# Optimization experiments

Measured on AMD Instinct MI355X. Metric: run time of the kernel, lower is better.

## Reference

```python
import jax, jax.numpy as jnp
import numpy as np

N, D_IN, D_HID, D_OUT = 16384, 512, 2048, 512
NUM_BANDS, RANK, ALPHA = 4, 16, 32
SCALING = ALPHA / RANK  # 2.0


def setup_inputs() -> dict:
    key = jax.random.key(0)
    ks = jax.random.split(key, 10)
    x = jax.random.normal(ks[0], (N, D_IN), dtype=jnp.float32)
    bw = jax.random.uniform(ks[1], (N, NUM_BANDS), dtype=jnp.float32)
    band_weights = bw / jnp.sum(bw, axis=-1, keepdims=True)  # rows sum to 1
    s_in = 1.0 / np.sqrt(D_IN)
    s_hid = 1.0 / np.sqrt(D_HID)
    return {
        "x": x,
        "band_weights": band_weights,
        "W1": jax.random.normal(ks[2], (D_IN, D_HID), dtype=jnp.float32) * s_in,
        "b1": jax.random.normal(ks[3], (D_HID,), dtype=jnp.float32) * 0.01,
        "W2": jax.random.normal(ks[4], (D_HID, D_OUT), dtype=jnp.float32) * s_hid,
        "b2": jax.random.normal(ks[5], (D_OUT,), dtype=jnp.float32) * 0.01,
        "lora_fc1_A": jax.random.normal(ks[6], (NUM_BANDS, D_IN, RANK), dtype=jnp.float32) * s_in,
        "lora_fc1_B": jax.random.normal(ks[7], (NUM_BANDS, RANK, D_HID), dtype=jnp.float32) * 0.02,
        "lora_fc2_A": jax.random.normal(ks[8], (NUM_BANDS, D_HID, RANK), dtype=jnp.float32) * s_hid,
        "lora_fc2_B": jax.random.normal(ks[9], (NUM_BANDS, RANK, D_OUT), dtype=jnp.float32) * 0.02,
    }


def reference(x, band_weights, W1, b1, W2, b2, lora_fc1_A, lora_fc1_B, lora_fc2_A, lora_fc2_B):
    # shared fc1: [N, hidden]
    h_shared = x @ W1 + b1
    # per-band LoRA down-projection: [N, bands, rank]
    t1 = jnp.einsum('ni,bir->nbr', x, lora_fc1_A)
    # up-project and band-weighted sum fused: [N, hidden]
    delta1 = jnp.einsum('nb,nbr,brh->nh', band_weights, t1, lora_fc1_B) * SCALING
    h = jax.nn.gelu(h_shared + delta1, approximate=False)  # torch GELU is erf-based
    out_shared = h @ W2 + b2
    t2 = jnp.einsum('nh,bhr->nbr', h, lora_fc2_A)
    delta2 = jnp.einsum('nb,nbr,bro->no', band_weights, t2, lora_fc2_B) * SCALING
    return out_shared + delta2
```

## Files before the change

### kernel.cpp

```cpp
#include <hip/hip_runtime.h>
#include <hip/hip_bf16.h>

#define DEV __device__ __forceinline__
#define AS1 __attribute__((address_space(1)))
#define AS3 __attribute__((address_space(3)))

typedef __attribute__((ext_vector_type(8))) short bf16x8;
typedef __attribute__((ext_vector_type(4))) float f32x4;

static constexpr int NR   = 16384;
static constexpr int DIN  = 512;
static constexpr int DHID = 2048;
static constexpr int DOUT = 512;
static constexpr int LR   = 64;
static constexpr int K1   = DIN + LR;
static constexpr int K2   = DHID + LR;

DEV unsigned short f2bf(float f) {
  unsigned u = __float_as_uint(f);
  u += 0x7fffu + ((u >> 16) & 1u);
  return (unsigned short)(u >> 16);
}

DEV float fast_gelu(float v) {
  float x2 = v * v;
  float a  = -v * __builtin_fmaf(0.10294324f, x2, 2.30220817f);
  float t  = exp2f(a);
  return v * __builtin_amdgcn_rcpf(1.0f + t);
}

template<int N> DEV void wvm() {
  asm volatile("s_waitcnt vmcnt(%0)" :: "i"(N) : "memory");
}

__global__ __launch_bounds__(256) void cvt_x_kernel(const float* __restrict__ x,
                                                    unsigned short* __restrict__ xaug) {
  int i = blockIdx.x * 256 + threadIdx.x;
  if (i >= NR * DIN / 4) return;
  int e = i * 4;
  int r = e >> 9, c = e & 511;
  float4 v = ((const float4*)x)[i];
  uint2 o;
  o.x = (unsigned)f2bf(v.x) | ((unsigned)f2bf(v.y) << 16);
  o.y = (unsigned)f2bf(v.z) | ((unsigned)f2bf(v.w) << 16);
  *(uint2*)(xaug + (size_t)r * K1 + c) = o;
}

template<int R, int C, int LDO, int CO>
__global__ __launch_bounds__(256) void tconv_kernel(const float* __restrict__ in,
                                                    unsigned short* __restrict__ out) {
  __shared__ float t[32][33];
  int bc = blockIdx.x * 32, br = blockIdx.y * 32;
  int tx = threadIdx.x & 31, ty = threadIdx.x >> 5;
  #pragma unroll
  for (int i = 0; i < 32; i += 8)
    t[ty + i][tx] = in[(size_t)(br + ty + i) * C + bc + tx];
  __syncthreads();
  #pragma unroll
  for (int i = 0; i < 32; i += 8)
    out[(size_t)(bc + ty + i) * LDO + CO + br + tx] = f2bf(t[tx][ty + i]);
}

__global__ __launch_bounds__(256) void rearrA_kernel(const float* __restrict__ A,
                                                     unsigned short* __restrict__ AT, int D) {
  int tid = blockIdx.x * 256 + threadIdx.x;
  if (tid >= 64 * D) return;
  int j = tid / D, i = tid - j * D;
  AT[tid] = f2bf(A[((size_t)(j >> 4) * D + i) * 16 + (j & 15)]);
}

template<int BM, int BN, int WAVES, int K, int EPI>
__global__ __launch_bounds__(WAVES * 64, 2) void gemm8_kernel(
    const unsigned short* __restrict__ A, int lda,
    const unsigned short* __restrict__ B, int ldb,
    const float* __restrict__ bias,
    void* __restrict__ outp, int ldo, int ocol) {
  constexpr int THREADS = WAVES * 64;
  constexpr int NT = K / 64;
  constexpr int AL = BM * 4 / THREADS;
  constexpr int BL = BN * 4 / THREADS;
  constexpr int HA = (BM / 2) * 64;
  constexpr int HB = (BN / 2) * 64;
  constexpr int MQ = BM / 64;
  constexpr int WC = WAVES / 2;
  static_assert(NT >= 2, "K tiles");
  __shared__ __align__(16) unsigned short lA[4 * HA];
  __shared__ __align__(16) unsigned short lB[4 * HB];

  const int tid  = threadIdx.x;
  const int w    = tid >> 6, lane = tid & 63;
  const int wr   = w / WC, wc = w % WC;
  const int bm   = blockIdx.x * BM, bn = blockIdx.y * BN;
  const int l15  = lane & 15;
  const int kc0  = ((lane >> 4) ^ (lane & 7)) * 8;
  const int kc1  = (((lane >> 4) + 4) ^ (lane & 7)) * 8;

  f32x4 acc[2][2][MQ][2] = {};
  bf16x8 af[MQ][2];
  bf16x8 bfv[2][2][2];

  auto stageA = [&](int buf, int half, int t) {
    #pragma unroll
    for (int i = 0; i < AL; ++i) {
      int row = w * (AL * 8) + i * 8 + (lane >> 3);
      __builtin_amdgcn_global_load_lds(
          (const AS1 void*)(A + (size_t)(bm + half * (BM / 2) + row) * lda
                              + (size_t)t * 64 + (((lane & 7) ^ (row & 7)) * 8)),
          (AS3 void*)(lA + (buf * 2 + half) * HA + (w * AL + i) * 512),
          16, 0, 0);
    }
  };
  auto stageB = [&](int buf, int half, int t) {
    #pragma unroll
    for (int i = 0; i < BL; ++i) {
      int row = w * (BL * 8) + i * 8 + (lane >> 3);
      __builtin_amdgcn_global_load_lds(
          (const AS1 void*)(B + (size_t)(bn + half * (BN / 2) + row) * ldb
                              + (size_t)t * 64 + (((lane & 7) ^ (row & 7)) * 8)),
          (AS3 void*)(lB + (buf * 2 + half) * HB + (w * BL + i) * 512),
          16, 0, 0);
    }
  };
  auto ldA = [&](int buf, int mh) {
    const unsigned short* sA = lA + (buf * 2 + mh) * HA;
    #pragma unroll
    for (int m = 0; m < MQ; ++m) {
      int ro = (wr * (BM / 4) + m * 16 + l15) * 64;
      af[m][0] = *(const bf16x8*)(sA + ro + kc0);
      af[m][1] = *(const bf16x8*)(sA + ro + kc1);
    }
  };
  auto ldB = [&](int buf, int nh) {
    const unsigned short* sB = lB + (buf * 2 + nh) * HB;
    #pragma unroll
    for (int n = 0; n < 2; ++n) {
      int ro = (wc * 32 + n * 16 + l15) * 64;
      bfv[nh][n][0] = *(const bf16x8*)(sB + ro + kc0);
      bfv[nh][n][1] = *(const bf16x8*)(sB + ro + kc1);
    }
  };

#define MFMA_Q(mh, nh)                                                           \
  __builtin_amdgcn_s_setprio(1);                                                 \
  _Pragma("unroll")                                                              \
  for (int m = 0; m < MQ; ++m)                                                   \
    _Pragma("unroll")                                                            \
    for (int n = 0; n < 2; ++n) {                                                \
      acc[mh][nh][m][n] = __builtin_amdgcn_mfma_f32_16x16x32_bf16(               \
          af[m][0], bfv[nh][n][0], acc[mh][nh][m][n], 0, 0, 0);                  \
      acc[mh][nh][m][n] = __builtin_amdgcn_mfma_f32_16x16x32_bf16(               \
          af[m][1], bfv[nh][n][1], acc[mh][nh][m][n], 0, 0, 0);                  \
    }                                                                            \
  __builtin_amdgcn_s_setprio(0);

  stageA(0, 0, 0); stageB(0, 0, 0); stageB(0, 1, 0); stageA(0, 1, 0);
  wvm<0>();
  __builtin_amdgcn_s_barrier();

  for (int t = 0; t < NT; ++t) {
    const int buf = t & 1, nb = buf ^ 1;
    const bool more = (t + 1 < NT);
    ldA(buf, 0);
    ldB(buf, 0);
    if (more) {
      stageA(nb, 0, t + 1); stageB(nb, 0, t + 1);
      stageB(nb, 1, t + 1); stageA(nb, 1, t + 1);
    }
    MFMA_Q(0, 0);
    ldB(buf, 1);
    MFMA_Q(0, 1);
    ldA(buf, 1);
    MFMA_Q(1, 1);
    MFMA_Q(1, 0);
    wvm<0>();
    __builtin_amdgcn_s_barrier();
  }
#undef MFMA_Q

  float biasv[2][2];
  #pragma unroll
  for (int nh = 0; nh < 2; ++nh)
    #pragma unroll
    for (int n = 0; n < 2; ++n)
      biasv[nh][n] = bias[bn + nh * (BN / 2) + wc * 32 + n * 16 + l15];

  #pragma unroll
  for (int mh = 0; mh < 2; ++mh)
    #pragma unroll
    for (int nh = 0; nh < 2; ++nh)
      #pragma unroll
      for (int m = 0; m < MQ; ++m)
        #pragma unroll
        for (int n = 0; n < 2; ++n) {
          int col  = bn + nh * (BN / 2) + wc * 32 + n * 16 + l15;
          int rowb = bm + mh * (BM / 2) + wr * (BM / 4) + m * 16 + ((lane >> 4) << 2);
          #pragma unroll
          for (int r = 0; r < 4; ++r) {
            float v = acc[mh][nh][m][n][r];
            int row = rowb + r;
            if (EPI == 0) {
              v = fast_gelu(v + biasv[nh][n]);
              ((unsigned short*)outp)[(size_t)row * ldo + ocol + col] = f2bf(v);
            } else {
              v += biasv[nh][n];
              ((float*)outp)[(size_t)row * ldo + col] = v;
            }
          }
        }
}

template<int BM, int BN, int WM, int WN, int K>
__global__ __launch_bounds__(256) void gemmu_kernel(
    const unsigned short* __restrict__ A, int lda,
    const unsigned short* __restrict__ B, int ldb,
    const float* __restrict__ bw,
    unsigned short* __restrict__ outp, int ldo, int ocol) {
  constexpr int WRM = WM / 16, WRN = WN / 16;
  constexpr int NWN = BN / WN;
  constexpr int NT  = K / 32;
  constexpr int NBUF = 3;
  constexpr int AISS = BM / 64;
  constexpr int BISS = BN / 64;
  constexpr int LOADS = AISS + BISS;
  static_assert((BM / WM) * (BN / WN) == 4, "4 waves");
  __shared__ __align__(16) unsigned short lA[NBUF * BM * 32];
  __shared__ __align__(16) unsigned short lB[NBUF * BN * 32];

  const int tid  = threadIdx.x;
  const int wid  = tid >> 6, lane = tid & 63;
  const int wr   = wid / NWN, wc = wid % NWN;
  const int bm   = blockIdx.x * BM, bn = blockIdx.y * BN;
  const int srow = lane >> 2;
  const int scol = (((lane & 3) ^ ((lane >> 2) & 3)) * 8);
  const int kch  = (((lane >> 4) ^ (lane & 3)) * 8);

  f32x4 acc[WRM][WRN] = {};

  auto stage = [&](int buf, int t) {
    #pragma unroll
    for (int i = 0; i < AISS; i++) {
      int row = i * 64 + wid * 16 + srow;
      __builtin_amdgcn_global_load_lds(
          (const AS1 void*)(A + (size_t)(bm + row) * lda + t * 32 + scol),
          (AS3 void*)(lA + buf * (BM * 32) + i * 2048 + wid * 512), 16, 0, 0);
    }
    #pragma unroll
    for (int i = 0; i < BISS; i++) {
      int row = i * 64 + wid * 16 + srow;
      __builtin_amdgcn_global_load_lds(
          (const AS1 void*)(B + (size_t)(bn + row) * ldb + t * 32 + scol),
          (AS3 void*)(lB + buf * (BN * 32) + i * 2048 + wid * 512), 16, 0, 0);
    }
  };
  auto compute = [&](int buf) {
    const unsigned short* pA = lA + buf * (BM * 32);
    const unsigned short* pB = lB + buf * (BN * 32);
    bf16x8 af[WRM], bfv[WRN];
    #pragma unroll
    for (int m = 0; m < WRM; m++)
      af[m] = *(const bf16x8*)(pA + (wr * WM + m * 16 + (lane & 15)) * 32 + kch);
    #pragma unroll
    for (int n = 0; n < WRN; n++)
      bfv[n] = *(const bf16x8*)(pB + (wc * WN + n * 16 + (lane & 15)) * 32 + kch);
    #pragma unroll
    for (int m = 0; m < WRM; m++)
      #pragma unroll
      for (int n = 0; n < WRN; n++)
        acc[m][n] = __builtin_amdgcn_mfma_f32_16x16x32_bf16(af[m], bfv[n], acc[m][n], 0, 0, 0);
  };

  stage(0, 0); stage(1, 1); stage(2, 2);
  wvm<2 * LOADS>();
  __builtin_amdgcn_s_barrier();

  int bt = 0;
  for (int t = 0; t < NT; ++t) {
    compute(bt);
    __builtin_amdgcn_s_barrier();
    if (t + 1 < NT) {
      if (t + NBUF < NT) stage(bt, t + NBUF);
      int newer = (t + NBUF < NT) ? (NBUF - 1) : (NT - 2 - t);
      if (newer >= 2)      wvm<2 * LOADS>();
      else if (newer == 1) wvm<LOADS>();
      else                 wvm<0>();
      __builtin_amdgcn_s_barrier();
      bt = (bt == NBUF - 1) ? 0 : bt + 1;
    }
  }

  const int r0 = bm + wr * WM;
  const int c0 = bn + wc * WN;
  #pragma unroll
  for (int m = 0; m < WRM; m++)
    #pragma unroll
    for (int n = 0; n < WRN; n++) {
      int col  = c0 + n * 16 + (lane & 15);
      int rowb = r0 + m * 16 + ((lane >> 4) << 2);
      #pragma unroll
      for (int r = 0; r < 4; r++) {
        float v = acc[m][n][r] * 2.0f * bw[(rowb + r) * 4 + (col >> 4)];
        outp[(size_t)(rowb + r) * ldo + ocol + col] = f2bf(v);
      }
    }
}

extern "C" void kernel_launch(void* const* d_in, const int* in_sizes, int n_in,
                              void* d_out, int out_size, void* d_ws, size_t ws_size,
                              hipStream_t stream) {
  const float* x  = (const float*)d_in[0];
  const float* bw = (const float*)d_in[1];
  const float* W1 = (const float*)d_in[2];
  const float* b1 = (const float*)d_in[3];
  const float* W2 = (const float*)d_in[4];
  const float* b2 = (const float*)d_in[5];
  const float* A1 = (const float*)d_in[6];
  const float* B1 = (const float*)d_in[7];
  const float* A2 = (const float*)d_in[8];
  const float* B2 = (const float*)d_in[9];
  float* out = (float*)d_out;

  char* w = (char*)d_ws;
  unsigned short* xaug = (unsigned short*)w;  w += (size_t)NR * K1 * 2;
  unsigned short* haug = (unsigned short*)w;  w += (size_t)NR * K2 * 2;
  unsigned short* W1cT = (unsigned short*)w;  w += (size_t)DHID * K1 * 2;
  unsigned short* W2cT = (unsigned short*)w;  w += (size_t)DOUT * K2 * 2;
  unsigned short* A1T  = (unsigned short*)w;  w += (size_t)64 * DIN * 2;
  unsigned short* A2T  = (unsigned short*)w;  w += (size_t)64 * DHID * 2;

  cvt_x_kernel<<<NR * DIN / 4 / 256, 256, 0, stream>>>(x, xaug);
  tconv_kernel<512, 2048, K1, 0><<<dim3(64, 16), 256, 0, stream>>>(W1, W1cT);
  tconv_kernel<64, 2048, K1, 512><<<dim3(64, 2), 256, 0, stream>>>(B1, W1cT);
  tconv_kernel<2048, 512, K2, 0><<<dim3(16, 64), 256, 0, stream>>>(W2, W2cT);
  tconv_kernel<64, 512, K2, 2048><<<dim3(16, 2), 256, 0, stream>>>(B2, W2cT);
  rearrA_kernel<<<128, 256, 0, stream>>>(A1, A1T, 512);
  rearrA_kernel<<<512, 256, 0, stream>>>(A2, A2T, 2048);

  gemmu_kernel<64, 64, 32, 32, 512><<<dim3(NR / 64, 1), 256, 0, stream>>>(
      xaug, K1, A1T, DIN, bw, xaug, K1, 512);
  gemm8_kernel<256, 256, 8, K1, 0><<<dim3(NR / 256, DHID / 256), 512, 0, stream>>>(
      xaug, K1, W1cT, K1, b1, haug, K2, 0);
  gemmu_kernel<64, 64, 32, 32, 2048><<<dim3(NR / 64, 1), 256, 0, stream>>>(
      haug, K2, A2T, DHID, bw, haug, K2, 2048);
  gemm8_kernel<128, 128, 4, K2, 1><<<dim3(NR / 128, DOUT / 128), 256, 0, stream>>>(
      haug, K2, W2cT, K2, b2, out, DOUT, 0);
}
```

Before: 147.3 us.

## Rework gemm8 into a finer-grained staged pipeline with 8 waves and 256-row tiles

The gemm8 kernel is restructured around a fixed 512-thread, 256-row block with a configurable wave grid (MW). The main loop is unrolled by two K tiles and interleaves half-tile global-to-LDS loads with the MFMA quadrants, using barriers between each phase. B for the next tile is prefetched early and waits are partial (vmcnt of 2*BL), so loads can overlap compute instead of waiting for everything each iteration. The fc2 GEMM moves from 128x128 tiles with 4 waves to 256x128 tiles with 8 waves, which doubles reuse of B per block but halves the block count and adds many more barriers.

```diff
diff --git a/kernel.cpp b/kernel.cpp
--- a/kernel.cpp
+++ b/kernel.cpp
@@ -69,42 +69,48 @@
   AT[tid] = f2bf(A[((size_t)(j >> 4) * D + i) * 16 + (j & 15)]);
 }
 
-template<int BM, int BN, int WAVES, int K, int EPI>
-__global__ __launch_bounds__(WAVES * 64, 2) void gemm8_kernel(
+template<int BM, int BN, int MW, int K, int EPI>
+__global__ __launch_bounds__(512, 2) void gemm8_kernel(
     const unsigned short* __restrict__ A, int lda,
     const unsigned short* __restrict__ B, int ldb,
     const float* __restrict__ bias,
     void* __restrict__ outp, int ldo, int ocol) {
-  constexpr int THREADS = WAVES * 64;
-  constexpr int NT = K / 64;
-  constexpr int AL = BM * 4 / THREADS;
-  constexpr int BL = BN * 4 / THREADS;
-  constexpr int HA = (BM / 2) * 64;
-  constexpr int HB = (BN / 2) * 64;
-  constexpr int MQ = BM / 64;
-  constexpr int WC = WAVES / 2;
-  static_assert(NT >= 2, "K tiles");
-  __shared__ __align__(16) unsigned short lA[4 * HA];
-  __shared__ __align__(16) unsigned short lB[4 * HB];
+  constexpr int NW  = 8 / MW;
+  constexpr int WMR = BM / MW, WNC = BN / NW;
+  constexpr int QR  = WMR / 2, QC = WNC / 2;
+  constexpr int MQ  = QR / 16, NQ = QC / 16;
+  constexpr int AL  = 2;
+  constexpr int BL  = BN / 128;
+  constexpr int HA  = 128 * 64;
+  constexpr int HB  = (BN / 2) * 64;
+  constexpr int NT  = K / 64;
+  constexpr int NJ  = NT / 2;
+  static_assert(BM == 256 && NT >= 3, "geometry");
+  __shared__ __align__(16) unsigned short lA[2 * 2 * HA];
+  __shared__ __align__(16) unsigned short lB[2 * 2 * HB];
 
   const int tid  = threadIdx.x;
   const int w    = tid >> 6, lane = tid & 63;
-  const int wr   = w / WC, wc = w % WC;
+  const int wr   = w / NW, wc = w % NW;
+  const int ah   = wr / (MW / 2);
+  const int rloc = (wr % (MW / 2)) * WMR;
+  const int bh   = wc / (NW / 2);
+  const int cloc = (wc % (NW / 2)) * WNC;
   const int bm   = blockIdx.x * BM, bn = blockIdx.y * BN;
   const int l15  = lane & 15;
   const int kc0  = ((lane >> 4) ^ (lane & 7)) * 8;
   const int kc1  = (((lane >> 4) + 4) ^ (lane & 7)) * 8;
 
-  f32x4 acc[2][2][MQ][2] = {};
+  f32x4 acc[2][2][MQ][NQ] = {};
   bf16x8 af[MQ][2];
-  bf16x8 bfv[2][2][2];
+  bf16x8 bfv[2][NQ][2];
 
   auto stageA = [&](int buf, int half, int t) {
     #pragma unroll
     for (int i = 0; i < AL; ++i) {
-      int row = w * (AL * 8) + i * 8 + (lane >> 3);
+      int row = (w * AL + i) * 8 + (lane >> 3);
       __builtin_amdgcn_global_load_lds(
-          (const AS1 void*)(A + (size_t)(bm + half * (BM / 2) + row) * lda
+          (const AS1 void*)(A + (size_t)(bm + half * 128 + row) * lda
                               + (size_t)t * 64 + (((lane & 7) ^ (row & 7)) * 8)),
           (AS3 void*)(lA + (buf * 2 + half) * HA + (w * AL + i) * 512),
           16, 0, 0);
@@ -113,7 +119,7 @@
   auto stageB = [&](int buf, int half, int t) {
     #pragma unroll
     for (int i = 0; i < BL; ++i) {
-      int row = w * (BL * 8) + i * 8 + (lane >> 3);
+      int row = (w * BL + i) * 8 + (lane >> 3);
       __builtin_amdgcn_global_load_lds(
           (const AS1 void*)(B + (size_t)(bn + half * (BN / 2) + row) * ldb
                               + (size_t)t * 64 + (((lane & 7) ^ (row & 7)) * 8)),
@@ -121,88 +127,127 @@
           16, 0, 0);
     }
   };
-  auto ldA = [&](int buf, int mh) {
-    const unsigned short* sA = lA + (buf * 2 + mh) * HA;
+  auto ldA = [&](int buf, int qm) {
+    const unsigned short* sA = lA + (buf * 2 + ah) * HA;
     #pragma unroll
     for (int m = 0; m < MQ; ++m) {
-      int ro = (wr * (BM / 4) + m * 16 + l15) * 64;
+      int ro = (rloc + qm * QR + m * 16 + l15) * 64;
       af[m][0] = *(const bf16x8*)(sA + ro + kc0);
       af[m][1] = *(const bf16x8*)(sA + ro + kc1);
     }
   };
-  auto ldB = [&](int buf, int nh) {
-    const unsigned short* sB = lB + (buf * 2 + nh) * HB;
-    #pragma unroll
-    for (int n = 0; n < 2; ++n) {
-      int ro = (wc * 32 + n * 16 + l15) * 64;
-      bfv[nh][n][0] = *(const bf16x8*)(sB + ro + kc0);
-      bfv[nh][n][1] = *(const bf16x8*)(sB + ro + kc1);
-    }
-  };
-
-#define MFMA_Q(mh, nh)                                                           \
+  auto ldB = [&](int buf, int qn) {
+    const unsigned short* sB = lB + (buf * 2 + bh) * HB;
+    #pragma unroll
+    for (int n = 0; n < NQ; ++n) {
+      int ro = (cloc + qn * QC + n * 16 + l15) * 64;
+      bfv[qn][n][0] = *(const bf16x8*)(sB + ro + kc0);
+      bfv[qn][n][1] = *(const bf16x8*)(sB + ro + kc1);
+    }
+  };
+
+#define MFMA_Q(qm, qn)                                                           \
   __builtin_amdgcn_s_setprio(1);                                                 \
   _Pragma("unroll")                                                              \
   for (int m = 0; m < MQ; ++m)                                                   \
     _Pragma("unroll")                                                            \
-    for (int n = 0; n < 2; ++n) {                                                \
-      acc[mh][nh][m][n] = __builtin_amdgcn_mfma_f32_16x16x32_bf16(               \
-          af[m][0], bfv[nh][n][0], acc[mh][nh][m][n], 0, 0, 0);                  \
-      acc[mh][nh][m][n] = __builtin_amdgcn_mfma_f32_16x16x32_bf16(               \
-          af[m][1], bfv[nh][n][1], acc[mh][nh][m][n], 0, 0, 0);                  \
+    for (int n = 0; n < NQ; ++n) {                                               \
+      acc[qm][qn][m][n] = __builtin_amdgcn_mfma_f32_16x16x32_bf16(               \
+          af[m][0], bfv[qn][n][0], acc[qm][qn][m][n], 0, 0, 0);                  \
+      acc[qm][qn][m][n] = __builtin_amdgcn_mfma_f32_16x16x32_bf16(               \
+          af[m][1], bfv[qn][n][1], acc[qm][qn][m][n], 0, 0, 0);                  \
     }                                                                            \
   __builtin_amdgcn_s_setprio(0);
 
-  stageA(0, 0, 0); stageB(0, 0, 0); stageB(0, 1, 0); stageA(0, 1, 0);
-  wvm<0>();
-  __builtin_amdgcn_s_barrier();
-
-  for (int t = 0; t < NT; ++t) {
-    const int buf = t & 1, nb = buf ^ 1;
-    const bool more = (t + 1 < NT);
-    ldA(buf, 0);
-    ldB(buf, 0);
-    if (more) {
-      stageA(nb, 0, t + 1); stageB(nb, 0, t + 1);
-      stageB(nb, 1, t + 1); stageA(nb, 1, t + 1);
-    }
+#define BAR() __builtin_amdgcn_s_barrier()
+
+  stageB(0, 0, 0); stageB(0, 1, 0); stageA(0, 0, 0); stageA(0, 1, 0);
+  stageB(1, 0, 1); stageB(1, 1, 1);
+  wvm<2 * BL>();
+  BAR();
+
+  for (int j = 0; j < NJ; ++j) {
+    const int T1 = 2 * j + 1, T2 = 2 * j + 2, T3 = 2 * j + 3;
+    ldA(0, 0); ldB(0, 0);
+    stageA(1, 0, T1);
+    BAR();
     MFMA_Q(0, 0);
-    ldB(buf, 1);
+    BAR();
+    ldB(0, 1);
+    stageA(1, 1, T1);
+    BAR();
     MFMA_Q(0, 1);
-    ldA(buf, 1);
+    BAR();
+    ldA(0, 1);
+    if (T2 < NT) stageB(0, 0, T2);
+    BAR();
+    MFMA_Q(1, 1);
+    BAR();
+    if (T2 < NT) stageB(0, 1, T2);
+    BAR();
+    MFMA_Q(1, 0);
+    if (T2 < NT) wvm<2 * BL>(); else wvm<0>();
+    BAR();
+    ldA(1, 0); ldB(1, 0);
+    if (T2 < NT) stageA(0, 0, T2);
+    BAR();
+    MFMA_Q(0, 0);
+    BAR();
+    ldB(1, 1);
+    if (T2 < NT) stageA(0, 1, T2);
+    BAR();
+    MFMA_Q(0, 1);
+    BAR();
+    ldA(1, 1);
+    if (T3 < NT) stageB(1, 0, T3);
+    BAR();
+    MFMA_Q(1, 1);
+    BAR();
+    if (T3 < NT) stageB(1, 1, T3);
+    BAR();
+    MFMA_Q(1, 0);
+    if (T3 < NT) wvm<2 * BL>(); else wvm<0>();
+    BAR();
+  }
+
+  if (NT & 1) {
+    ldA(0, 0); ldB(0, 0);
+    MFMA_Q(0, 0);
+    ldB(0, 1);
+    MFMA_Q(0, 1);
+    ldA(0, 1);
     MFMA_Q(1, 1);
     MFMA_Q(1, 0);
-    wvm<0>();
-    __builtin_amdgcn_s_barrier();
   }
 #undef MFMA_Q
-
-  float biasv[2][2];
-  #pragma unroll
-  for (int nh = 0; nh < 2; ++nh)
-    #pragma unroll
-    for (int n = 0; n < 2; ++n)
-      biasv[nh][n] = bias[bn + nh * (BN / 2) + wc * 32 + n * 16 + l15];
-
-  #pragma unroll
-  for (int mh = 0; mh < 2; ++mh)
-    #pragma unroll
-    for (int nh = 0; nh < 2; ++nh)
+#undef BAR
+
+  float biasv[2][NQ];
+  #pragma unroll
+  for (int qn = 0; qn < 2; ++qn)
+    #pragma unroll
+    for (int n = 0; n < NQ; ++n)
+      biasv[qn][n] = bias[bn + bh * (BN / 2) + cloc + qn * QC + n * 16 + l15];
+
+  #pragma unroll
+  for (int qm = 0; qm < 2; ++qm)
+    #pragma unroll
+    for (int qn = 0; qn < 2; ++qn)
       #pragma unroll
       for (int m = 0; m < MQ; ++m)
         #pragma unroll
-        for (int n = 0; n < 2; ++n) {
-          int col  = bn + nh * (BN / 2) + wc * 32 + n * 16 + l15;
-          int rowb = bm + mh * (BM / 2) + wr * (BM / 4) + m * 16 + ((lane >> 4) << 2);
+        for (int n = 0; n < NQ; ++n) {
+          int col  = bn + bh * (BN / 2) + cloc + qn * QC + n * 16 + l15;
+          int rowb = bm + ah * 128 + rloc + qm * QR + m * 16 + ((lane >> 4) << 2);
           #pragma unroll
           for (int r = 0; r < 4; ++r) {
-            float v = acc[mh][nh][m][n][r];
+            float v = acc[qm][qn][m][n][r];
             int row = rowb + r;
             if (EPI == 0) {
-              v = fast_gelu(v + biasv[nh][n]);
+              v = fast_gelu(v + biasv[qn][n]);
               ((unsigned short*)outp)[(size_t)row * ldo + ocol + col] = f2bf(v);
             } else {
-              v += biasv[nh][n];
+              v += biasv[qn][n];
               ((float*)outp)[(size_t)row * ldo + col] = v;
             }
           }
@@ -337,10 +382,10 @@
 
   gemmu_kernel<64, 64, 32, 32, 512><<<dim3(NR / 64, 1), 256, 0, stream>>>(
       xaug, K1, A1T, DIN, bw, xaug, K1, 512);
-  gemm8_kernel<256, 256, 8, K1, 0><<<dim3(NR / 256, DHID / 256), 512, 0, stream>>>(
+  gemm8_kernel<256, 256, 2, K1, 0><<<dim3(NR / 256, DHID / 256), 512, 0, stream>>>(
       xaug, K1, W1cT, K1, b1, haug, K2, 0);
   gemmu_kernel<64, 64, 32, 32, 2048><<<dim3(NR / 64, 1), 256, 0, stream>>>(
       haug, K2, A2T, DHID, bw, haug, K2, 2048);
-  gemm8_kernel<128, 128, 4, K2, 1><<<dim3(NR / 128, DOUT / 128), 256, 0, stream>>>(
+  gemm8_kernel<256, 128, 4, K2, 1><<<dim3(NR / 256, DOUT / 128), 512, 0, stream>>>(
       haug, K2, W2cT, K2, b2, out, DOUT, 0);
 }
```

New measurement: 150.6 us. +2.2%, slower.

## Split main GEMM K-loop into two barrier phases and widen LoRA GEMM K-tile

Applied to the files above, without the earlier changes.

The main GEMM loop now loads all A fragments up front and computes the nh=0 quadrants first. Partial vmcnt waits and a mid-iteration barrier let the last B half-tile be staged later, so global-to-LDS loads overlap more with MFMA work instead of draining at the end of each tile. The LoRA down-projection GEMM moves from 32-wide to 64-wide K tiles with an XOR-swizzled LDS layout, giving two MFMAs per fragment pair and half as many pipeline iterations. This costs more registers for A fragments and twice the LDS for the triple-buffered LoRA kernel, which may reduce occupancy.

```diff
diff --git a/kernel.cpp b/kernel.cpp
--- a/kernel.cpp
+++ b/kernel.cpp
@@ -70,7 +70,7 @@
 }
 
 template<int BM, int BN, int WAVES, int K, int EPI>
-__global__ __launch_bounds__(WAVES * 64, 2) void gemm8_kernel(
+__global__ __launch_bounds__(WAVES * 64, 2) void gemmx_kernel(
     const unsigned short* __restrict__ A, int lda,
     const unsigned short* __restrict__ B, int ldb,
     const float* __restrict__ bias,
@@ -83,7 +83,7 @@
   constexpr int HB = (BN / 2) * 64;
   constexpr int MQ = BM / 64;
   constexpr int WC = WAVES / 2;
-  static_assert(NT >= 2, "K tiles");
+  static_assert(NT >= 2 && AL == 2 && BL == 2, "geometry");
   __shared__ __align__(16) unsigned short lA[4 * HA];
   __shared__ __align__(16) unsigned short lB[4 * HB];
 
@@ -96,8 +96,8 @@
   const int kc1  = (((lane >> 4) + 4) ^ (lane & 7)) * 8;
 
   f32x4 acc[2][2][MQ][2] = {};
-  bf16x8 af[MQ][2];
-  bf16x8 bfv[2][2][2];
+  bf16x8 af[2][MQ][2];
+  bf16x8 bfv[2][2];
 
   auto stageA = [&](int buf, int half, int t) {
     #pragma unroll
@@ -121,13 +121,16 @@
           16, 0, 0);
     }
   };
-  auto ldA = [&](int buf, int mh) {
-    const unsigned short* sA = lA + (buf * 2 + mh) * HA;
-    #pragma unroll
-    for (int m = 0; m < MQ; ++m) {
-      int ro = (wr * (BM / 4) + m * 16 + l15) * 64;
-      af[m][0] = *(const bf16x8*)(sA + ro + kc0);
-      af[m][1] = *(const bf16x8*)(sA + ro + kc1);
+  auto ldAall = [&](int buf) {
+    #pragma unroll
+    for (int mh = 0; mh < 2; ++mh) {
+      const unsigned short* sA = lA + (buf * 2 + mh) * HA;
+      #pragma unroll
+      for (int m = 0; m < MQ; ++m) {
+        int ro = (wr * (BM / 4) + m * 16 + l15) * 64;
+        af[mh][m][0] = *(const bf16x8*)(sA + ro + kc0);
+        af[mh][m][1] = *(const bf16x8*)(sA + ro + kc1);
+      }
     }
   };
   auto ldB = [&](int buf, int nh) {
@@ -135,8 +138,8 @@
     #pragma unroll
     for (int n = 0; n < 2; ++n) {
       int ro = (wc * 32 + n * 16 + l15) * 64;
-      bfv[nh][n][0] = *(const bf16x8*)(sB + ro + kc0);
-      bfv[nh][n][1] = *(const bf16x8*)(sB + ro + kc1);
+      bfv[n][0] = *(const bf16x8*)(sB + ro + kc0);
+      bfv[n][1] = *(const bf16x8*)(sB + ro + kc1);
     }
   };
 
@@ -147,35 +150,39 @@
     _Pragma("unroll")                                                            \
     for (int n = 0; n < 2; ++n) {                                                \
       acc[mh][nh][m][n] = __builtin_amdgcn_mfma_f32_16x16x32_bf16(               \
-          af[m][0], bfv[nh][n][0], acc[mh][nh][m][n], 0, 0, 0);                  \
+          af[mh][m][0], bfv[n][0], acc[mh][nh][m][n], 0, 0, 0);                  \
       acc[mh][nh][m][n] = __builtin_amdgcn_mfma_f32_16x16x32_bf16(               \
-          af[m][1], bfv[nh][n][1], acc[mh][nh][m][n], 0, 0, 0);                  \
+          af[mh][m][1], bfv[n][1], acc[mh][nh][m][n], 0, 0, 0);                  \
     }                                                                            \
   __builtin_amdgcn_s_setprio(0);
 
-  stageA(0, 0, 0); stageB(0, 0, 0); stageB(0, 1, 0); stageA(0, 1, 0);
-  wvm<0>();
-  __builtin_amdgcn_s_barrier();
+#define BAR() __builtin_amdgcn_s_barrier()
+
+  stageA(0, 0, 0); stageA(0, 1, 0); stageB(0, 0, 0); stageB(0, 1, 0);
+  wvm<2>();
+  BAR();
 
   for (int t = 0; t < NT; ++t) {
     const int buf = t & 1, nb = buf ^ 1;
     const bool more = (t + 1 < NT);
-    ldA(buf, 0);
+    ldAall(buf);
     ldB(buf, 0);
-    if (more) {
-      stageA(nb, 0, t + 1); stageB(nb, 0, t + 1);
-      stageB(nb, 1, t + 1); stageA(nb, 1, t + 1);
-    }
+    if (more) { stageA(nb, 0, t + 1); stageA(nb, 1, t + 1); stageB(nb, 0, t + 1); }
     MFMA_Q(0, 0);
+    MFMA_Q(1, 0);
+    if (more) wvm<6>(); else wvm<0>();
+    BAR();
+    if (more) stageB(nb, 1, t + 1);
     ldB(buf, 1);
     MFMA_Q(0, 1);
-    ldA(buf, 1);
     MFMA_Q(1, 1);
-    MFMA_Q(1, 0);
-    wvm<0>();
-    __builtin_amdgcn_s_barrier();
+    if (more) {
+      wvm<2>();
+      BAR();
+    }
   }
 #undef MFMA_Q
+#undef BAR
 
   float biasv[2][2];
   #pragma unroll
@@ -217,56 +224,66 @@
     unsigned short* __restrict__ outp, int ldo, int ocol) {
   constexpr int WRM = WM / 16, WRN = WN / 16;
   constexpr int NWN = BN / WN;
-  constexpr int NT  = K / 32;
+  constexpr int NT  = K / 64;
   constexpr int NBUF = 3;
-  constexpr int AISS = BM / 64;
-  constexpr int BISS = BN / 64;
+  constexpr int AISS = BM * 64 * 2 / 4096;
+  constexpr int BISS = BN * 64 * 2 / 4096;
   constexpr int LOADS = AISS + BISS;
-  static_assert((BM / WM) * (BN / WN) == 4, "4 waves");
-  __shared__ __align__(16) unsigned short lA[NBUF * BM * 32];
-  __shared__ __align__(16) unsigned short lB[NBUF * BN * 32];
+  static_assert((BM / WM) * (BN / WN) == 4 && NT >= NBUF, "geometry");
+  __shared__ __align__(16) unsigned short lA[NBUF * BM * 64];
+  __shared__ __align__(16) unsigned short lB[NBUF * BN * 64];
 
   const int tid  = threadIdx.x;
   const int wid  = tid >> 6, lane = tid & 63;
   const int wr   = wid / NWN, wc = wid % NWN;
   const int bm   = blockIdx.x * BM, bn = blockIdx.y * BN;
-  const int srow = lane >> 2;
-  const int scol = (((lane & 3) ^ ((lane >> 2) & 3)) * 8);
-  const int kch  = (((lane >> 4) ^ (lane & 3)) * 8);
+  const int l15  = lane & 15;
+  const int kc0  = ((lane >> 4) ^ (lane & 7)) * 8;
+  const int kc1  = (((lane >> 4) + 4) ^ (lane & 7)) * 8;
 
   f32x4 acc[WRM][WRN] = {};
 
   auto stage = [&](int buf, int t) {
     #pragma unroll
     for (int i = 0; i < AISS; i++) {
-      int row = i * 64 + wid * 16 + srow;
+      int row = (wid * AISS + i) * 8 + (lane >> 3);
       __builtin_amdgcn_global_load_lds(
-          (const AS1 void*)(A + (size_t)(bm + row) * lda + t * 32 + scol),
-          (AS3 void*)(lA + buf * (BM * 32) + i * 2048 + wid * 512), 16, 0, 0);
+          (const AS1 void*)(A + (size_t)(bm + row) * lda + (size_t)t * 64
+                              + (((lane & 7) ^ (row & 7)) * 8)),
+          (AS3 void*)(lA + buf * (BM * 64) + (wid * AISS + i) * 512), 16, 0, 0);
     }
     #pragma unroll
     for (int i = 0; i < BISS; i++) {
-      int row = i * 64 + wid * 16 + srow;
+      int row = (wid * BISS + i) * 8 + (lane >> 3);
       __builtin_amdgcn_global_load_lds(
-          (const AS1 void*)(B + (size_t)(bn + row) * ldb + t * 32 + scol),
-          (AS3 void*)(lB + buf * (BN * 32) + i * 2048 + wid * 512), 16, 0, 0);
+          (const AS1 void*)(B + (size_t)(bn + row) * ldb + (size_t)t * 64
+                              + (((lane & 7) ^ (row & 7)) * 8)),
+          (AS3 void*)(lB + buf * (BN * 64) + (wid * BISS + i) * 512), 16, 0, 0);
     }
   };
   auto compute = [&](int buf) {
-    const unsigned short* pA = lA + buf * (BM * 32);
-    const unsigned short* pB = lB + buf * (BN * 32);
-    bf16x8 af[WRM], bfv[WRN];
-    #pragma unroll
-    for (int m = 0; m < WRM; m++)
-      af[m] = *(const bf16x8*)(pA + (wr * WM + m * 16 + (lane & 15)) * 32 + kch);
-    #pragma unroll
-    for (int n = 0; n < WRN; n++)
-      bfv[n] = *(const bf16x8*)(pB + (wc * WN + n * 16 + (lane & 15)) * 32 + kch);
+    const unsigned short* pA = lA + buf * (BM * 64);
+    const unsigned short* pB = lB + buf * (BN * 64);
+    bf16x8 af[WRM][2], bfv[WRN][2];
+    #pragma unroll
+    for (int m = 0; m < WRM; m++) {
+      int ro = (wr * WM + m * 16 + l15) * 64;
+      af[m][0] = *(const bf16x8*)(pA + ro + kc0);
+      af[m][1] = *(const bf16x8*)(pA + ro + kc1);
+    }
+    #pragma unroll
+    for (int n = 0; n < WRN; n++) {
+      int ro = (wc * WN + n * 16 + l15) * 64;
+      bfv[n][0] = *(const bf16x8*)(pB + ro + kc0);
+      bfv[n][1] = *(const bf16x8*)(pB + ro + kc1);
+    }
     #pragma unroll
     for (int m = 0; m < WRM; m++)
       #pragma unroll
-      for (int n = 0; n < WRN; n++)
-        acc[m][n] = __builtin_amdgcn_mfma_f32_16x16x32_bf16(af[m], bfv[n], acc[m][n], 0, 0, 0);
+      for (int n = 0; n < WRN; n++) {
+        acc[m][n] = __builtin_amdgcn_mfma_f32_16x16x32_bf16(af[m][0], bfv[n][0], acc[m][n], 0, 0, 0);
+        acc[m][n] = __builtin_amdgcn_mfma_f32_16x16x32_bf16(af[m][1], bfv[n][1], acc[m][n], 0, 0, 0);
+      }
   };
 
   stage(0, 0); stage(1, 1); stage(2, 2);
@@ -294,7 +311,7 @@
   for (int m = 0; m < WRM; m++)
     #pragma unroll
     for (int n = 0; n < WRN; n++) {
-      int col  = c0 + n * 16 + (lane & 15);
+      int col  = c0 + n * 16 + l15;
       int rowb = r0 + m * 16 + ((lane >> 4) << 2);
       #pragma unroll
       for (int r = 0; r < 4; r++) {
@@ -337,10 +354,10 @@
 
   gemmu_kernel<64, 64, 32, 32, 512><<<dim3(NR / 64, 1), 256, 0, stream>>>(
       xaug, K1, A1T, DIN, bw, xaug, K1, 512);
-  gemm8_kernel<256, 256, 8, K1, 0><<<dim3(NR / 256, DHID / 256), 512, 0, stream>>>(
+  gemmx_kernel<256, 256, 8, K1, 0><<<dim3(NR / 256, DHID / 256), 512, 0, stream>>>(
       xaug, K1, W1cT, K1, b1, haug, K2, 0);
   gemmu_kernel<64, 64, 32, 32, 2048><<<dim3(NR / 64, 1), 256, 0, stream>>>(
       haug, K2, A2T, DHID, bw, haug, K2, 2048);
-  gemm8_kernel<128, 128, 4, K2, 1><<<dim3(NR / 128, DOUT / 128), 256, 0, stream>>>(
+  gemmx_kernel<128, 128, 4, K2, 1><<<dim3(NR / 128, DOUT / 128), 256, 0, stream>>>(
       haug, K2, W2cT, K2, b2, out, DOUT, 0);
 }
```

Result: no change. 145.0 us (-1.6%).
